# Kernel optimization log

Hardware: AMD Instinct MI355X
Metric: run time of the kernel (lower is better)

Reference implementation:

```python
import jax, jax.numpy as jnp
import numpy as np

DIM = 768
HEADS = 12
HEAD_DIM = DIM // HEADS


def setup_inputs() -> dict:
    key = jax.random.key(0)
    ks = jax.random.split(key, 5)
    B, N = 2, 2048
    x = jax.random.normal(ks[0], (B, N, DIM), dtype=jnp.float32)
    s = 1.0 / np.sqrt(DIM)
    qkv_w = jax.random.normal(ks[1], (3 * DIM, DIM), dtype=jnp.float32) * s
    qkv_b = jnp.zeros((3 * DIM,), dtype=jnp.float32)
    proj_w = jax.random.normal(ks[2], (DIM, DIM), dtype=jnp.float32) * s
    proj_b = jnp.zeros((DIM,), dtype=jnp.float32)
    return {"x": x, "qkv_w": qkv_w, "qkv_b": qkv_b, "proj_w": proj_w, "proj_b": proj_b}


def reference(x, qkv_w, qkv_b, proj_w, proj_b):
    B, N, C = x.shape
    scale = HEAD_DIM ** -0.5
    qkv = x @ qkv_w.T + qkv_b                      # [B,N,3C]
    qkv = qkv.reshape(B, N, 3, HEADS, HEAD_DIM)
    q = qkv[:, :, 0].transpose(0, 2, 1, 3)         # [B,H,N,D]
    k = qkv[:, :, 1].transpose(0, 2, 1, 3)
    v = qkv[:, :, 2].transpose(0, 2, 1, 3)
    attn = jnp.einsum('bhnd,bhmd->bhnm', q, k) * scale
    attn = jax.nn.softmax(attn, axis=-1)
    out = jnp.einsum('bhnm,bhmd->bhnd', attn, v)   # [B,H,N,D]
    out = out.transpose(0, 2, 1, 3).reshape(B, N, C)
    return out @ proj_w.T + proj_b
```

## Files before the change

kernel.cpp:

```cpp
#include <hip/hip_runtime.h>
#include <hip/hip_bf16.h>

typedef __bf16 bf16x8 __attribute__((ext_vector_type(8)));
typedef float f32x4 __attribute__((ext_vector_type(4)));
typedef float f32x16 __attribute__((ext_vector_type(16)));

#define SEQ   2048
#define NHEAD 12
#define NBH   24
#define QSCALE 0.18033688011112042f

#define CP16(g, l) __builtin_amdgcn_global_load_lds( \
    (const __attribute__((address_space(1))) unsigned int*)(g), \
    (__attribute__((address_space(3))) unsigned int*)(l), 16, 0, 0)

__device__ __forceinline__ unsigned short f2bf(float f) {
  unsigned int u = __builtin_bit_cast(unsigned int, f);
  u += 0x7FFFu + ((u >> 16) & 1u);
  return (unsigned short)(u >> 16);
}
__device__ __forceinline__ float bfu2f(unsigned int lo16_as_hi) {
  return __builtin_bit_cast(float, lo16_as_hi);
}
__device__ __forceinline__ unsigned int packbf2_trunc(float lo, float hi) {
  return __builtin_amdgcn_perm(__builtin_bit_cast(unsigned int, hi),
                               __builtin_bit_cast(unsigned int, lo), 0x07060302u);
}

#define NX4  786432
#define NW14 442368
__global__ __launch_bounds__(256) void cvt3_kernel(const float4* __restrict__ x,
                                                   const float4* __restrict__ w1,
                                                   const float4* __restrict__ w2,
                                                   ushort4* __restrict__ xo,
                                                   ushort4* __restrict__ w1o,
                                                   ushort4* __restrict__ w2o) {
  int i = blockIdx.x * 256 + threadIdx.x;
  const float4* s;
  ushort4* d;
  int j = i;
  if (i < NX4)               { s = x;  d = xo; }
  else if (i < NX4 + NW14)   { s = w1; d = w1o; j = i - NX4; }
  else                       { s = w2; d = w2o; j = i - (NX4 + NW14); }
  float4 v = s[j];
  ushort4 r;
  r.x = f2bf(v.x); r.y = f2bf(v.y); r.z = f2bf(v.z); r.w = f2bf(v.w);
  d[j] = r;
}

template <int BM, int BN, int MODE>
__global__ __launch_bounds__(256) void gemm_kernel(const unsigned short* __restrict__ X,
                                                   const unsigned short* __restrict__ W,
                                                   const float* __restrict__ bias,
                                                   unsigned short* __restrict__ Qb,
                                                   unsigned short* __restrict__ Kb,
                                                   unsigned short* __restrict__ Vtb,
                                                   float* __restrict__ Out) {
  constexpr int K = 768, BK = 64, NKT = K / BK;
  constexpr int WM = BM / 2, WN = BN / 2;
  constexpr int MT = WM / 16, NT = WN / 16;
  __shared__ __align__(16) unsigned short Xs[2][BM * BK];
  __shared__ __align__(16) unsigned short Ws[2][BN * BK];

  const int tid = threadIdx.x;
  const int w = tid >> 6, lane = tid & 63, quad = lane >> 4, m16 = lane & 15;
  const int wm = w & 1, wn = w >> 1;
  const int row0 = blockIdx.y * BM, col0 = blockIdx.x * BN;

  f32x4 acc[MT][NT];
#pragma unroll
  for (int mt = 0; mt < MT; ++mt)
#pragma unroll
    for (int nt = 0; nt < NT; ++nt) acc[mt][nt] = (f32x4){0.f, 0.f, 0.f, 0.f};

#pragma unroll
  for (int j = 0; j < BM / 32; ++j) {
    int e = tid + 256 * j, r = e >> 3, c8 = e & 7;
    CP16(X + (size_t)(row0 + r) * 768 + ((c8 ^ (r & 7)) << 3), &Xs[0][e * 8]);
  }
#pragma unroll
  for (int j = 0; j < BN / 32; ++j) {
    int e = tid + 256 * j, r = e >> 3, c8 = e & 7;
    CP16(W + (size_t)(col0 + r) * 768 + ((c8 ^ (r & 7)) << 3), &Ws[0][e * 8]);
  }

#pragma unroll 2
  for (int kt = 0; kt < NKT; ++kt) {
    const int cur = kt & 1;
    __syncthreads();

    bf16x8 a[2][MT], b[2][NT];
#pragma unroll
    for (int ks = 0; ks < 2; ++ks) {
      const int sw = ((quad + 4 * ks) ^ (m16 & 7)) << 3;
#pragma unroll
      for (int mt = 0; mt < MT; ++mt)
        a[ks][mt] = *(const bf16x8*)(&Xs[cur][(wm * WM + mt * 16 + m16) * BK + sw]);
#pragma unroll
      for (int nt = 0; nt < NT; ++nt)
        b[ks][nt] = *(const bf16x8*)(&Ws[cur][(wn * WN + nt * 16 + m16) * BK + sw]);
    }

    if (kt < NKT - 1) {
      const int k0n = (kt + 1) * BK, nb = 1 - cur;
#pragma unroll
      for (int j = 0; j < BM / 32; ++j) {
        int e = tid + 256 * j, r = e >> 3, c8 = e & 7;
        CP16(X + (size_t)(row0 + r) * 768 + k0n + ((c8 ^ (r & 7)) << 3), &Xs[nb][e * 8]);
      }
#pragma unroll
      for (int j = 0; j < BN / 32; ++j) {
        int e = tid + 256 * j, r = e >> 3, c8 = e & 7;
        CP16(W + (size_t)(col0 + r) * 768 + k0n + ((c8 ^ (r & 7)) << 3), &Ws[nb][e * 8]);
      }
    }

#pragma unroll
    for (int ks = 0; ks < 2; ++ks)
#pragma unroll
      for (int mt = 0; mt < MT; ++mt)
#pragma unroll
        for (int nt = 0; nt < NT; ++nt)
          acc[mt][nt] = __builtin_amdgcn_mfma_f32_16x16x32_bf16(a[ks][mt], b[ks][nt], acc[mt][nt], 0, 0, 0);
  }

#pragma unroll
  for (int mt = 0; mt < MT; ++mt) {
#pragma unroll
    for (int nt = 0; nt < NT; ++nt) {
      const int m0 = row0 + wm * WM + mt * 16 + quad * 4;
      const int c = col0 + wn * WN + nt * 16 + m16;
      const float bia = bias[c];
      f32x4 v = acc[mt][nt];
      if constexpr (MODE == 0) {
        const int bidx = m0 >> 11, ns = m0 & 2047;
        if (c < 1536) {
          unsigned short* dst;
          float sc;
          int cc;
          if (c < 768) { cc = c; dst = Qb; sc = QSCALE; }
          else         { cc = c - 768; dst = Kb; sc = 1.0f; }
          const int h = cc >> 6, d = cc & 63;
          unsigned short* p = dst + ((size_t)(bidx * NHEAD + h) * SEQ + ns) * 64 + d;
          p[0]   = f2bf((v[0] + bia) * sc);
          p[64]  = f2bf((v[1] + bia) * sc);
          p[128] = f2bf((v[2] + bia) * sc);
          p[192] = f2bf((v[3] + bia) * sc);
        } else {
          const int cc = c - 1536, h = cc >> 6, d = cc & 63;
          const int ns2 = (ns & ~12) | ((ns & 4) << 1) | ((ns & 8) >> 1);
          ushort4 pk;
          pk.x = f2bf(v[0] + bia); pk.y = f2bf(v[1] + bia);
          pk.z = f2bf(v[2] + bia); pk.w = f2bf(v[3] + bia);
          *(ushort4*)(Vtb + ((size_t)(bidx * NHEAD + h) * 64 + d) * SEQ + ns2) = pk;
        }
      } else {
        float* o = Out + (size_t)m0 * 768 + c;
        o[0]       = v[0] + bia;
        o[768]     = v[1] + bia;
        o[2 * 768] = v[2] + bia;
        o[3 * 768] = v[3] + bia;
      }
    }
  }
}

__global__ __launch_bounds__(128) void attn_kernel(const unsigned short* __restrict__ Qb,
                                                   const unsigned short* __restrict__ Kb,
                                                   const unsigned short* __restrict__ Vtb,
                                                   unsigned short* __restrict__ O0,
                                                   unsigned short* __restrict__ O1,
                                                   float2* __restrict__ ml) {
  __shared__ __align__(16) unsigned short Ks[2][64 * 64];
  __shared__ __align__(16) unsigned short Vts[2][64 * 64];

  const int tid = threadIdx.x;
  const int w = tid >> 6, lane = tid & 63, hi = lane >> 5, l32 = lane & 31;
  const int bh = blockIdx.x % NBH;
  const int rest = blockIdx.x / NBH;
  const int qt = rest & 31, half = rest >> 5;
  const int bb = bh / NHEAD, h = bh % NHEAD;
  const int q0 = qt * 64 + w * 32;

  const unsigned short* Qp = Qb + (size_t)bh * SEQ * 64;
  const unsigned short* Kp = Kb + (size_t)bh * SEQ * 64 + (size_t)half * 16 * 4096;
  const unsigned short* Vp = Vtb + (size_t)bh * 64 * SEQ + half * 1024;

  bf16x8 qf[4];
#pragma unroll
  for (int dc = 0; dc < 4; ++dc)
    qf[dc] = *(const bf16x8*)(Qp + (size_t)(q0 + l32) * 64 + dc * 16 + hi * 8);

#pragma unroll
  for (int j = 0; j < 4; ++j) {
    int e = tid + 128 * j, r = e >> 3, c8 = e & 7;
    CP16(Kp + (size_t)r * 64 + ((c8 ^ (r & 7)) << 3), &Ks[0][e * 8]);
    CP16(Vp + (size_t)r * SEQ + ((c8 ^ (r & 7)) << 3), &Vts[0][e * 8]);
  }

  f32x16 o[2] = {};
  float m_i = -3.0e38f, l_i = 0.f;

  for (int kt = 0; kt < 16; ++kt) {
    const int cur = kt & 1;
    __syncthreads();

    const unsigned short* Kc = Ks[cur];
    const unsigned short* Vc = Vts[cur];
    bf16x8 kf[2][4], vf[2][4];
#pragma unroll
    for (int t32 = 0; t32 < 2; ++t32)
#pragma unroll
      for (int dc = 0; dc < 4; ++dc)
        kf[t32][dc] = *(const bf16x8*)(Kc + (t32 * 32 + l32) * 64 + ((((dc << 1) | hi) ^ (l32 & 7)) << 3));
#pragma unroll
    for (int dt = 0; dt < 2; ++dt)
#pragma unroll
      for (int cc = 0; cc < 4; ++cc)
        vf[dt][cc] = *(const bf16x8*)(Vc + (dt * 32 + l32) * 64 + ((((cc << 1) | hi) ^ (l32 & 7)) << 3));

    if (kt < 15) {
      const int kn = kt + 1, nb = 1 - cur;
#pragma unroll
      for (int j = 0; j < 4; ++j) {
        int e = tid + 128 * j, r = e >> 3, c8 = e & 7;
        CP16(Kp + (size_t)(kn * 64 + r) * 64 + ((c8 ^ (r & 7)) << 3), &Ks[nb][e * 8]);
        CP16(Vp + (size_t)r * SEQ + kn * 64 + ((c8 ^ (r & 7)) << 3), &Vts[nb][e * 8]);
      }
    }

    f32x16 st[2];
#pragma unroll
    for (int t32 = 0; t32 < 2; ++t32) {
      f32x16 s = {};
#pragma unroll
      for (int dc = 0; dc < 4; ++dc)
        s = __builtin_amdgcn_mfma_f32_32x32x16_bf16(kf[t32][dc], qf[dc], s, 0, 0, 0);
      st[t32] = s;
    }

    float tmax = st[0][0];
#pragma unroll
    for (int t32 = 0; t32 < 2; ++t32)
#pragma unroll
      for (int e = 0; e < 16; ++e) tmax = fmaxf(tmax, st[t32][e]);
    tmax = fmaxf(tmax, __shfl_xor(tmax, 32));
    const float mnew = fmaxf(m_i, tmax);
    const float alpha = __builtin_amdgcn_exp2f(m_i - mnew);
    float ssum = 0.f;
    unsigned int pf[2][8];
#pragma unroll
    for (int t32 = 0; t32 < 2; ++t32) {
      float pv[16];
#pragma unroll
      for (int e = 0; e < 16; ++e) { pv[e] = __builtin_amdgcn_exp2f(st[t32][e] - mnew); ssum += pv[e]; }
#pragma unroll
      for (int e2 = 0; e2 < 8; ++e2)
        pf[t32][e2] = packbf2_trunc(pv[2 * e2], pv[2 * e2 + 1]);
    }
    ssum += __shfl_xor(ssum, 32);
    l_i = l_i * alpha + ssum;
    m_i = mnew;
    o[0] *= alpha;
    o[1] *= alpha;

#pragma unroll
    for (int t32 = 0; t32 < 2; ++t32) {
#pragma unroll
      for (int hh = 0; hh < 2; ++hh) {
        bf16x8 pfrag = __builtin_bit_cast(bf16x8,
            make_uint4(pf[t32][hh * 4], pf[t32][hh * 4 + 1], pf[t32][hh * 4 + 2], pf[t32][hh * 4 + 3]));
        const int cc = 2 * t32 + hh;
#pragma unroll
        for (int dt = 0; dt < 2; ++dt)
          o[dt] = __builtin_amdgcn_mfma_f32_32x32x16_bf16(vf[dt][cc], pfrag, o[dt], 0, 0, 0);
      }
    }
  }

  unsigned short* base = (half ? O1 : O0) + ((size_t)bb * SEQ + q0 + l32) * 768 + h * 64;
#pragma unroll
  for (int dt = 0; dt < 2; ++dt) {
#pragma unroll
    for (int run = 0; run < 4; ++run) {
      ushort4 pk;
      pk.x = f2bf(o[dt][run * 4 + 0]);
      pk.y = f2bf(o[dt][run * 4 + 1]);
      pk.z = f2bf(o[dt][run * 4 + 2]);
      pk.w = f2bf(o[dt][run * 4 + 3]);
      *(ushort4*)(base + dt * 32 + run * 8 + hi * 4) = pk;
    }
  }
  if (hi == 0)
    ml[(size_t)half * (NBH * SEQ) + bh * SEQ + q0 + l32] = make_float2(m_i, l_i);
}

__global__ __launch_bounds__(256) void combine_kernel(unsigned short* __restrict__ O0,
                                                      const unsigned short* __restrict__ O1,
                                                      const float2* __restrict__ ml) {
  const int gid = blockIdx.x * 256 + threadIdx.x;
  const int t = gid / 48, ci = gid - t * 48;
  const int ch0 = ci * 16, h = ch0 >> 6;
  const int mlrow = ((t >> 11) * NHEAD + h) * SEQ + (t & 2047);
  const float2 ml0 = ml[mlrow], ml1 = ml[NBH * SEQ + mlrow];
  const float m = fmaxf(ml0.x, ml1.x);
  const float a0 = __builtin_amdgcn_exp2f(ml0.x - m);
  const float a1 = __builtin_amdgcn_exp2f(ml1.x - m);
  const float rl = __builtin_amdgcn_rcpf(a0 * ml0.y + a1 * ml1.y);
  const float s0 = a0 * rl, s1 = a1 * rl;
  unsigned short* p0 = O0 + (size_t)t * 768 + ch0;
  const unsigned short* p1 = O1 + (size_t)t * 768 + ch0;
  uint4 x[2], y[2];
  x[0] = *(const uint4*)p0;       x[1] = *(const uint4*)(p0 + 8);
  y[0] = *(const uint4*)p1;       y[1] = *(const uint4*)(p1 + 8);
#pragma unroll
  for (int q = 0; q < 2; ++q) {
    unsigned int* xu = (unsigned int*)&x[q];
    const unsigned int* yu = (const unsigned int*)&y[q];
#pragma unroll
    for (int e = 0; e < 4; ++e) {
      const unsigned int u0 = xu[e], u1 = yu[e];
      const float lo = bfu2f(u0 << 16) * s0 + bfu2f(u1 << 16) * s1;
      const float hi = bfu2f(u0 & 0xFFFF0000u) * s0 + bfu2f(u1 & 0xFFFF0000u) * s1;
      xu[e] = ((unsigned int)f2bf(hi) << 16) | f2bf(lo);
    }
  }
  *(uint4*)p0 = x[0];
  *(uint4*)(p0 + 8) = x[1];
}

extern "C" void kernel_launch(void* const* d_in, const int* in_sizes, int n_in,
                              void* d_out, int out_size, void* d_ws, size_t ws_size,
                              hipStream_t stream) {
  const float* x      = (const float*)d_in[0];
  const float* qkv_w  = (const float*)d_in[1];
  const float* qkv_b  = (const float*)d_in[2];
  const float* proj_w = (const float*)d_in[3];
  const float* proj_b = (const float*)d_in[4];
  float* out = (float*)d_out;

  unsigned short* xb  = (unsigned short*)d_ws;
  unsigned short* wqb = xb + 3145728;
  unsigned short* wpb = wqb + 1769472;
  unsigned short* Qb  = wpb + 589824;
  unsigned short* Kb  = Qb + 3145728;
  unsigned short* Vtb = Kb + 3145728;
  unsigned short* Ab  = Vtb + 3145728;

  cvt3_kernel<<<5376, 256, 0, stream>>>((const float4*)x, (const float4*)qkv_w, (const float4*)proj_w,
                                        (ushort4*)xb, (ushort4*)wqb, (ushort4*)wpb);
  gemm_kernel<128, 96, 0><<<dim3(24, 32), 256, 0, stream>>>(xb, wqb, qkv_b, Qb, Kb, Vtb, nullptr);
  attn_kernel<<<1536, 128, 0, stream>>>(Qb, Kb, Vtb, Ab, xb, (float2*)wqb);
  combine_kernel<<<768, 256, 0, stream>>>(Ab, xb, (const float2*)wqb);
  gemm_kernel<64, 96, 1><<<dim3(8, 64), 256, 0, stream>>>(Ab, wpb, proj_b, nullptr, nullptr, nullptr, out);
}
```

Before: 173.0 us.

## Drop GEMM double buffering, shrink QKV tile, widen attention blocks to four waves

The GEMM kernel drops its double-buffered LDS prefetch in favour of single-buffer load, sync, compute steps. It gains a thread-count template parameter, and the QKV projection tile shrinks from 128 to 64 rows, doubling the grid. The attention kernel moves to 256 threads covering 128 query rows per block, so each K/V tile loaded into LDS is shared by four waves instead of two. The aim is less LDS per block, higher occupancy and more K/V reuse, but GEMM global loads no longer overlap with MFMA compute.

After: 162.5 us. -6.0%, faster.

```diff
diff --git a/kernel.cpp b/kernel.cpp
--- a/kernel.cpp
+++ b/kernel.cpp
@@ -48,19 +48,20 @@
   d[j] = r;
 }
 
-template <int BM, int BN, int MODE>
-__global__ __launch_bounds__(256) void gemm_kernel(const unsigned short* __restrict__ X,
+template <int BM, int BN, int NTH, int MODE>
+__global__ __launch_bounds__(NTH) void gemm_kernel(const unsigned short* __restrict__ X,
                                                    const unsigned short* __restrict__ W,
                                                    const float* __restrict__ bias,
                                                    unsigned short* __restrict__ Qb,
                                                    unsigned short* __restrict__ Kb,
                                                    unsigned short* __restrict__ Vtb,
                                                    float* __restrict__ Out) {
-  constexpr int K = 768, BK = 64, NKT = K / BK;
-  constexpr int WM = BM / 2, WN = BN / 2;
+  constexpr int K = 768, BK = 64;
+  constexpr int WAVES_N = (NTH / 64) / 2;
+  constexpr int WM = BM / 2, WN = BN / WAVES_N;
   constexpr int MT = WM / 16, NT = WN / 16;
-  __shared__ __align__(16) unsigned short Xs[2][BM * BK];
-  __shared__ __align__(16) unsigned short Ws[2][BN * BK];
+  __shared__ __align__(16) unsigned short Xs[BM * BK];
+  __shared__ __align__(16) unsigned short Ws[BN * BK];
 
   const int tid = threadIdx.x;
   const int w = tid >> 6, lane = tid & 63, quad = lane >> 4, m16 = lane & 15;
@@ -73,55 +74,35 @@
 #pragma unroll
     for (int nt = 0; nt < NT; ++nt) acc[mt][nt] = (f32x4){0.f, 0.f, 0.f, 0.f};
 
-#pragma unroll
-  for (int j = 0; j < BM / 32; ++j) {
-    int e = tid + 256 * j, r = e >> 3, c8 = e & 7;
-    CP16(X + (size_t)(row0 + r) * 768 + ((c8 ^ (r & 7)) << 3), &Xs[0][e * 8]);
-  }
-#pragma unroll
-  for (int j = 0; j < BN / 32; ++j) {
-    int e = tid + 256 * j, r = e >> 3, c8 = e & 7;
-    CP16(W + (size_t)(col0 + r) * 768 + ((c8 ^ (r & 7)) << 3), &Ws[0][e * 8]);
-  }
-
-#pragma unroll 2
-  for (int kt = 0; kt < NKT; ++kt) {
-    const int cur = kt & 1;
+  for (int k0 = 0; k0 < K; k0 += BK) {
     __syncthreads();
-
-    bf16x8 a[2][MT], b[2][NT];
+#pragma unroll
+    for (int j = 0; j < BM * 8 / NTH; ++j) {
+      int e = tid + NTH * j, r = e >> 3, c8 = e & 7;
+      CP16(X + (size_t)(row0 + r) * 768 + k0 + ((c8 ^ (r & 7)) << 3), Xs + e * 8);
+    }
+#pragma unroll
+    for (int j = 0; j < BN * 8 / NTH; ++j) {
+      int e = tid + NTH * j, r = e >> 3, c8 = e & 7;
+      CP16(W + (size_t)(col0 + r) * 768 + k0 + ((c8 ^ (r & 7)) << 3), Ws + e * 8);
+    }
+    __syncthreads();
 #pragma unroll
     for (int ks = 0; ks < 2; ++ks) {
       const int sw = ((quad + 4 * ks) ^ (m16 & 7)) << 3;
+      bf16x8 a[MT], b[NT];
 #pragma unroll
       for (int mt = 0; mt < MT; ++mt)
-        a[ks][mt] = *(const bf16x8*)(&Xs[cur][(wm * WM + mt * 16 + m16) * BK + sw]);
+        a[mt] = *(const bf16x8*)(Xs + (wm * WM + mt * 16 + m16) * BK + sw);
 #pragma unroll
       for (int nt = 0; nt < NT; ++nt)
-        b[ks][nt] = *(const bf16x8*)(&Ws[cur][(wn * WN + nt * 16 + m16) * BK + sw]);
-    }
-
-    if (kt < NKT - 1) {
-      const int k0n = (kt + 1) * BK, nb = 1 - cur;
-#pragma unroll
-      for (int j = 0; j < BM / 32; ++j) {
-        int e = tid + 256 * j, r = e >> 3, c8 = e & 7;
-        CP16(X + (size_t)(row0 + r) * 768 + k0n + ((c8 ^ (r & 7)) << 3), &Xs[nb][e * 8]);
-      }
-#pragma unroll
-      for (int j = 0; j < BN / 32; ++j) {
-        int e = tid + 256 * j, r = e >> 3, c8 = e & 7;
-        CP16(W + (size_t)(col0 + r) * 768 + k0n + ((c8 ^ (r & 7)) << 3), &Ws[nb][e * 8]);
-      }
-    }
-
-#pragma unroll
-    for (int ks = 0; ks < 2; ++ks)
+        b[nt] = *(const bf16x8*)(Ws + (wn * WN + nt * 16 + m16) * BK + sw);
 #pragma unroll
       for (int mt = 0; mt < MT; ++mt)
 #pragma unroll
         for (int nt = 0; nt < NT; ++nt)
-          acc[mt][nt] = __builtin_amdgcn_mfma_f32_16x16x32_bf16(a[ks][mt], b[ks][nt], acc[mt][nt], 0, 0, 0);
+          acc[mt][nt] = __builtin_amdgcn_mfma_f32_16x16x32_bf16(a[mt], b[nt], acc[mt][nt], 0, 0, 0);
+    }
   }
 
 #pragma unroll
@@ -165,7 +146,7 @@
   }
 }
 
-__global__ __launch_bounds__(128) void attn_kernel(const unsigned short* __restrict__ Qb,
+__global__ __launch_bounds__(256) void attn_kernel(const unsigned short* __restrict__ Qb,
                                                    const unsigned short* __restrict__ Kb,
                                                    const unsigned short* __restrict__ Vtb,
                                                    unsigned short* __restrict__ O0,
@@ -178,9 +159,9 @@
   const int w = tid >> 6, lane = tid & 63, hi = lane >> 5, l32 = lane & 31;
   const int bh = blockIdx.x % NBH;
   const int rest = blockIdx.x / NBH;
-  const int qt = rest & 31, half = rest >> 5;
+  const int qt = rest & 15, half = rest >> 4;
   const int bb = bh / NHEAD, h = bh % NHEAD;
-  const int q0 = qt * 64 + w * 32;
+  const int q0 = qt * 128 + w * 32;
 
   const unsigned short* Qp = Qb + (size_t)bh * SEQ * 64;
   const unsigned short* Kp = Kb + (size_t)bh * SEQ * 64 + (size_t)half * 16 * 4096;
@@ -192,8 +173,8 @@
     qf[dc] = *(const bf16x8*)(Qp + (size_t)(q0 + l32) * 64 + dc * 16 + hi * 8);
 
 #pragma unroll
-  for (int j = 0; j < 4; ++j) {
-    int e = tid + 128 * j, r = e >> 3, c8 = e & 7;
+  for (int j = 0; j < 2; ++j) {
+    int e = tid + 256 * j, r = e >> 3, c8 = e & 7;
     CP16(Kp + (size_t)r * 64 + ((c8 ^ (r & 7)) << 3), &Ks[0][e * 8]);
     CP16(Vp + (size_t)r * SEQ + ((c8 ^ (r & 7)) << 3), &Vts[0][e * 8]);
   }
@@ -222,8 +203,8 @@
     if (kt < 15) {
       const int kn = kt + 1, nb = 1 - cur;
 #pragma unroll
-      for (int j = 0; j < 4; ++j) {
-        int e = tid + 128 * j, r = e >> 3, c8 = e & 7;
+      for (int j = 0; j < 2; ++j) {
+        int e = tid + 256 * j, r = e >> 3, c8 = e & 7;
         CP16(Kp + (size_t)(kn * 64 + r) * 64 + ((c8 ^ (r & 7)) << 3), &Ks[nb][e * 8]);
         CP16(Vp + (size_t)r * SEQ + kn * 64 + ((c8 ^ (r & 7)) << 3), &Vts[nb][e * 8]);
       }
@@ -349,8 +330,8 @@
 
   cvt3_kernel<<<5376, 256, 0, stream>>>((const float4*)x, (const float4*)qkv_w, (const float4*)proj_w,
                                         (ushort4*)xb, (ushort4*)wqb, (ushort4*)wpb);
-  gemm_kernel<128, 96, 0><<<dim3(24, 32), 256, 0, stream>>>(xb, wqb, qkv_b, Qb, Kb, Vtb, nullptr);
-  attn_kernel<<<1536, 128, 0, stream>>>(Qb, Kb, Vtb, Ab, xb, (float2*)wqb);
+  gemm_kernel<64, 96, 256, 0><<<dim3(24, 64), 256, 0, stream>>>(xb, wqb, qkv_b, Qb, Kb, Vtb, nullptr);
+  attn_kernel<<<768, 256, 0, stream>>>(Qb, Kb, Vtb, Ab, xb, (float2*)wqb);
   combine_kernel<<<768, 256, 0, stream>>>(Ab, xb, (const float2*)wqb);
-  gemm_kernel<64, 96, 1><<<dim3(8, 64), 256, 0, stream>>>(Ab, wpb, proj_b, nullptr, nullptr, nullptr, out);
-}
+  gemm_kernel<64, 96, 256, 1><<<dim3(8, 64), 256, 0, stream>>>(Ab, wpb, proj_b, nullptr, nullptr, nullptr, out);
+}
```
